# Optimization experiments

Hardware: AMD Instinct MI355X
Metric: run time of the kernel (lower is better)

## Reference

```python
import math
import jax, jax.numpy as jnp
import numpy as np

EPS = 1e-6
M, B, K, D, DZ = 4, 2048, 32, 256, 128

def setup_inputs() -> dict:
    key = jax.random.key(0)
    ks = jax.random.split(key, 8)
    return {
        "h_nei": jax.random.normal(ks[0], (M, B, K, D), jnp.float32),
        "ew_anc": jax.random.uniform(ks[1], (B, K, M), jnp.float32),
        "view_mask": jnp.ones((B, K, M), jnp.float32),
        "z_anc": jax.random.normal(ks[2], (B, DZ), jnp.float32),
        "lbl_delta": jax.random.normal(ks[3], (B, K, M, D), jnp.float32),
        "lbl_weight": jax.random.normal(ks[4], (B, K, M), jnp.float32) * 0.1,
        "W_Q": jax.random.normal(ks[5], (DZ, D), jnp.float32) / math.sqrt(DZ),
        "W_K": jax.random.normal(ks[6], (M, D, D), jnp.float32) / math.sqrt(D),
        "W_V": jax.random.normal(ks[7], (M, D, D), jnp.float32) / math.sqrt(D),
        "log_vw": jnp.zeros((M,), jnp.float32),
    }

def reference(h_nei, ew_anc, view_mask, z_anc, lbl_delta, lbl_weight, W_Q, W_K, W_V, log_vw):
    # Cross-attention mode (use_query_z=True). Dropout is identity (eval mode).
    d = h_nei.shape[-1]
    Q = z_anc @ W_Q                                            # [B, d]
    Kx = jnp.einsum('mbkd,mde->mbke', h_nei, W_K)              # [M, B, K, d]
    Vx = jnp.einsum('mbkd,mde->mbke', h_nei, W_V)
    Vx = Vx + jnp.moveaxis(lbl_delta, 2, 0)                    # add lbl_delta[:,:,m,:]
    ew = jnp.moveaxis(ew_anc, 2, 0)                            # [M, B, K]
    lw = jnp.moveaxis(lbl_weight, 2, 0)
    vm = jnp.moveaxis(view_mask, 2, 0)
    scores = jnp.einsum('bd,mbkd->mbk', Q, Kx) / math.sqrt(d)
    scores = scores + jnp.log(ew + EPS) + lw
    scores = jnp.where(vm == 0, -1e9, scores)
    attn = jax.nn.softmax(scores, axis=-1)                     # [M, B, K]
    ctx_m = jnp.einsum('mbk,mbkd->mbd', attn, Vx)              # [M, B, d]
    vw = jax.nn.softmax(log_vw)                                # [M]
    return jnp.einsum('m,mbd->bd', vw, ctx_m)                  # [B, d]
```

## Files before the change

kernel.cpp:

```cpp
#include <hip/hip_runtime.h>
#include <hip/hip_bf16.h>
#include <math.h>

#define M_  4
#define B_  2048
#define K_  32
#define D_  256
#define DZ_ 128
#define PAD 68

__global__ void __launch_bounds__(256) k0_wqk(const float* __restrict__ W_Q,
                                              const float* __restrict__ W_K,
                                              float* __restrict__ Wqk) {
    int mz = blockIdx.x;
    int m = mz >> 7, z = mz & 127;
    int d = threadIdx.x;
    __shared__ float wq[D_];
    wq[d] = W_Q[z * D_ + d];
    __syncthreads();
    const float* wk = W_K + (m * D_ + d) * D_;
    float acc = 0.f;
#pragma unroll 8
    for (int e = 0; e < D_; ++e) acc = fmaf(wq[e], wk[e], acc);
    Wqk[(m * DZ_ + z) * D_ + d] = acc;
}

__global__ void __launch_bounds__(256) k1_qk(const float* __restrict__ z_anc,
                                             const float* __restrict__ Wqk,
                                             float* __restrict__ Qk) {
    int m = blockIdx.z;
    int b0 = blockIdx.x * 64, d0 = blockIdx.y * 64;
    int t = threadIdx.x, tx = t & 15, ty = t >> 4;
    __shared__ float As[64 * PAD];
    __shared__ float Bs[64 * PAD];
    float c[4][4] = {};
    for (int kc = 0; kc < DZ_; kc += 64) {
#pragma unroll
        for (int it = 0; it < 4; ++it) {
            int s = it * 256 + t, bi = s >> 4, k4 = (s & 15) * 4;
            *(float4*)&As[bi * PAD + k4] =
                *(const float4*)&z_anc[(b0 + bi) * DZ_ + kc + k4];
        }
#pragma unroll
        for (int it = 0; it < 4; ++it) {
            int s = it * 256 + t, kk = s >> 4, d4 = (s & 15) * 4;
            *(float4*)&Bs[kk * PAD + d4] =
                *(const float4*)&Wqk[(m * DZ_ + kc + kk) * D_ + d0 + d4];
        }
        __syncthreads();
#pragma unroll 4
        for (int kk = 0; kk < 64; ++kk) {
            float a[4];
#pragma unroll
            for (int i = 0; i < 4; ++i) a[i] = As[(ty * 4 + i) * PAD + kk];
            float4 b4 = *(const float4*)&Bs[kk * PAD + tx * 4];
#pragma unroll
            for (int i = 0; i < 4; ++i) {
                c[i][0] = fmaf(a[i], b4.x, c[i][0]);
                c[i][1] = fmaf(a[i], b4.y, c[i][1]);
                c[i][2] = fmaf(a[i], b4.z, c[i][2]);
                c[i][3] = fmaf(a[i], b4.w, c[i][3]);
            }
        }
        __syncthreads();
    }
#pragma unroll
    for (int i = 0; i < 4; ++i) {
        float4 v = make_float4(c[i][0], c[i][1], c[i][2], c[i][3]);
        *(float4*)&Qk[(m * B_ + b0 + ty * 4 + i) * D_ + d0 + tx * 4] = v;
    }
}

__global__ void __launch_bounds__(256) k2_main(
    const float* __restrict__ h_nei, const float* __restrict__ ew_anc,
    const float* __restrict__ vmask, const float* __restrict__ lbl_delta,
    const float* __restrict__ lbl_w, const float* __restrict__ Qk,
    const float* __restrict__ log_vw,
    float* __restrict__ hbar, float* __restrict__ out)
{
    int b = blockIdx.x;
    int t = threadIdx.x;
    int w = t >> 6, l = t & 63;
    __shared__ float hs[K_ * D_];
    __shared__ float sc[K_], adj[K_], at[K_];

    float lv[4] = {log_vw[0], log_vw[1], log_vw[2], log_vw[3]};
    float mv = fmaxf(fmaxf(lv[0], lv[1]), fmaxf(lv[2], lv[3]));
    float ex[4], den = 0.f;
#pragma unroll
    for (int i = 0; i < 4; ++i) { ex[i] = expf(lv[i] - mv); den += ex[i]; }
    float vw[4];
#pragma unroll
    for (int i = 0; i < 4; ++i) vw[i] = ex[i] / den;

    float acc_ld = 0.f;
    for (int m = 0; m < M_; ++m) {
        __syncthreads();
        const float* hb = h_nei + (m * B_ + b) * (K_ * D_);
        float4 q4 = *(const float4*)&Qk[(m * B_ + b) * D_ + 4 * l];
        float accs[8];
#pragma unroll
        for (int i = 0; i < 8; ++i) {
            int s = i * 256 + t;
            float4 h4 = *(const float4*)&hb[4 * s];
            *(float4*)&hs[4 * s] = h4;
            accs[i] = h4.x * q4.x + h4.y * q4.y + h4.z * q4.z + h4.w * q4.w;
        }
#pragma unroll
        for (int i = 0; i < 8; ++i) {
            float v = accs[i];
            v += __shfl_xor(v, 32); v += __shfl_xor(v, 16); v += __shfl_xor(v, 8);
            v += __shfl_xor(v, 4);  v += __shfl_xor(v, 2);  v += __shfl_xor(v, 1);
            if (l == 0) sc[i * 4 + w] = v;
        }
        __syncthreads();
        if (t < K_) {
            int idx = (b * K_ + t) * M_ + m;
            float s = sc[t] * 0.0625f + logf(ew_anc[idx] + 1e-6f) + lbl_w[idx];
            if (vmask[idx] == 0.f) s = -1e9f;
            adj[t] = s;
        }
        __syncthreads();
        float mx = -3.4e38f;
        for (int k = 0; k < K_; ++k) mx = fmaxf(mx, adj[k]);
        float dsum = 0.f;
        for (int k = 0; k < K_; ++k) dsum += expf(adj[k] - mx);
        if (t < K_) at[t] = expf(adj[t] - mx) / dsum;
        __syncthreads();
        float ah = 0.f;
#pragma unroll 8
        for (int k = 0; k < K_; ++k) ah = fmaf(at[k], hs[k * D_ + t], ah);
        hbar[(m * B_ + b) * D_ + t] = vw[m] * ah;
        const float* ldp = lbl_delta + b * (K_ * M_ * D_) + m * D_;
        float vwm = vw[m];
#pragma unroll 8
        for (int k = 0; k < K_; ++k)
            acc_ld = fmaf(vwm * at[k], ldp[k * (M_ * D_) + t], acc_ld);
    }
    out[b * D_ + t] = acc_ld;
}

__global__ void __launch_bounds__(256) k3_gemm(const float* __restrict__ hbar,
                                               const float* __restrict__ W_V,
                                               float* __restrict__ out) {
    int m = blockIdx.z;
    int b0 = blockIdx.x * 64, e0 = blockIdx.y * 64;
    int t = threadIdx.x, tx = t & 15, ty = t >> 4;
    __shared__ float As[64 * PAD];
    __shared__ float Bs[64 * PAD];
    float c[4][4] = {};
    for (int kc = 0; kc < D_; kc += 64) {
#pragma unroll
        for (int it = 0; it < 4; ++it) {
            int s = it * 256 + t, bi = s >> 4, k4 = (s & 15) * 4;
            *(float4*)&As[bi * PAD + k4] =
                *(const float4*)&hbar[(m * B_ + b0 + bi) * D_ + kc + k4];
        }
#pragma unroll
        for (int it = 0; it < 4; ++it) {
            int s = it * 256 + t, kk = s >> 4, e4 = (s & 15) * 4;
            *(float4*)&Bs[kk * PAD + e4] =
                *(const float4*)&W_V[(m * D_ + kc + kk) * D_ + e0 + e4];
        }
        __syncthreads();
#pragma unroll 4
        for (int kk = 0; kk < 64; ++kk) {
            float a[4];
#pragma unroll
            for (int i = 0; i < 4; ++i) a[i] = As[(ty * 4 + i) * PAD + kk];
            float4 b4 = *(const float4*)&Bs[kk * PAD + tx * 4];
#pragma unroll
            for (int i = 0; i < 4; ++i) {
                c[i][0] = fmaf(a[i], b4.x, c[i][0]);
                c[i][1] = fmaf(a[i], b4.y, c[i][1]);
                c[i][2] = fmaf(a[i], b4.z, c[i][2]);
                c[i][3] = fmaf(a[i], b4.w, c[i][3]);
            }
        }
        __syncthreads();
    }
#pragma unroll
    for (int i = 0; i < 4; ++i)
#pragma unroll
        for (int j = 0; j < 4; ++j)
            atomicAdd(&out[(b0 + ty * 4 + i) * D_ + e0 + tx * 4 + j], c[i][j]);
}

extern "C" void kernel_launch(void* const* d_in, const int* in_sizes, int n_in,
                              void* d_out, int out_size, void* d_ws, size_t ws_size,
                              hipStream_t stream) {
    const float* h_nei     = (const float*)d_in[0];
    const float* ew_anc    = (const float*)d_in[1];
    const float* vmask     = (const float*)d_in[2];
    const float* z_anc     = (const float*)d_in[3];
    const float* lbl_delta = (const float*)d_in[4];
    const float* lbl_w     = (const float*)d_in[5];
    const float* W_Q       = (const float*)d_in[6];
    const float* W_K       = (const float*)d_in[7];
    const float* W_V       = (const float*)d_in[8];
    const float* log_vw    = (const float*)d_in[9];
    float* out = (float*)d_out;

    float* ws   = (float*)d_ws;
    float* Wqk  = ws;
    float* Qk   = ws + (M_ * DZ_ * D_);
    float* hbar = ws + (M_ * DZ_ * D_) + (M_ * B_ * D_);

    k0_wqk<<<M_ * DZ_, 256, 0, stream>>>(W_Q, W_K, Wqk);

    dim3 g1(B_ / 64, D_ / 64, M_);
    k1_qk<<<g1, 256, 0, stream>>>(z_anc, Wqk, Qk);

    k2_main<<<B_, 256, 0, stream>>>(h_nei, ew_anc, vmask, lbl_delta, lbl_w,
                                    Qk, log_vw, hbar, out);

    dim3 g3(B_ / 64, D_ / 64, M_);
    k3_gemm<<<g3, 256, 0, stream>>>(hbar, W_V, out);
}
```

Measured before the change: 189.8 us.

## Split main kernel across views, keep neighbor tile in registers, relayout hbar

After: 219.2 us. 1.16x slower.

```diff
diff --git a/kernel.cpp b/kernel.cpp
--- a/kernel.cpp
+++ b/kernel.cpp
@@ -78,89 +78,104 @@
     const float* __restrict__ log_vw,
     float* __restrict__ hbar, float* __restrict__ out)
 {
-    int b = blockIdx.x;
+    int b = blockIdx.x, m = blockIdx.y;
     int t = threadIdx.x;
     int w = t >> 6, l = t & 63;
-    __shared__ float hs[K_ * D_];
-    __shared__ float sc[K_], adj[K_], at[K_];
-
-    float lv[4] = {log_vw[0], log_vw[1], log_vw[2], log_vw[3]};
-    float mv = fmaxf(fmaxf(lv[0], lv[1]), fmaxf(lv[2], lv[3]));
-    float ex[4], den = 0.f;
-#pragma unroll
-    for (int i = 0; i < 4; ++i) { ex[i] = expf(lv[i] - mv); den += ex[i]; }
-    float vw[4];
-#pragma unroll
-    for (int i = 0; i < 4; ++i) vw[i] = ex[i] / den;
-
-    float acc_ld = 0.f;
-    for (int m = 0; m < M_; ++m) {
-        __syncthreads();
-        const float* hb = h_nei + (m * B_ + b) * (K_ * D_);
-        float4 q4 = *(const float4*)&Qk[(m * B_ + b) * D_ + 4 * l];
-        float accs[8];
-#pragma unroll
-        for (int i = 0; i < 8; ++i) {
-            int s = i * 256 + t;
-            float4 h4 = *(const float4*)&hb[4 * s];
-            *(float4*)&hs[4 * s] = h4;
-            accs[i] = h4.x * q4.x + h4.y * q4.y + h4.z * q4.z + h4.w * q4.w;
-        }
-#pragma unroll
-        for (int i = 0; i < 8; ++i) {
-            float v = accs[i];
-            v += __shfl_xor(v, 32); v += __shfl_xor(v, 16); v += __shfl_xor(v, 8);
-            v += __shfl_xor(v, 4);  v += __shfl_xor(v, 2);  v += __shfl_xor(v, 1);
-            if (l == 0) sc[i * 4 + w] = v;
-        }
-        __syncthreads();
-        if (t < K_) {
-            int idx = (b * K_ + t) * M_ + m;
-            float s = sc[t] * 0.0625f + logf(ew_anc[idx] + 1e-6f) + lbl_w[idx];
-            if (vmask[idx] == 0.f) s = -1e9f;
-            adj[t] = s;
-        }
-        __syncthreads();
-        float mx = -3.4e38f;
-        for (int k = 0; k < K_; ++k) mx = fmaxf(mx, adj[k]);
-        float dsum = 0.f;
-        for (int k = 0; k < K_; ++k) dsum += expf(adj[k] - mx);
-        if (t < K_) at[t] = expf(adj[t] - mx) / dsum;
-        __syncthreads();
-        float ah = 0.f;
+    __shared__ float sc[K_];
+    __shared__ float at[K_];
+    __shared__ float part[4 * D_];
+
+    float lv0 = log_vw[0], lv1 = log_vw[1], lv2 = log_vw[2], lv3 = log_vw[3];
+    float mv = fmaxf(fmaxf(lv0, lv1), fmaxf(lv2, lv3));
+    float e0 = expf(lv0 - mv), e1 = expf(lv1 - mv),
+          e2 = expf(lv2 - mv), e3 = expf(lv3 - mv);
+    float vw_m = ((m == 0) ? e0 : (m == 1) ? e1 : (m == 2) ? e2 : e3)
+                 / (e0 + e1 + e2 + e3);
+
+    float adjv = 0.f, vmv = 1.f;
+    if (t < K_) {
+        int idx = (b * K_ + t) * M_ + m;
+        adjv = logf(ew_anc[idx] + 1e-6f) + lbl_w[idx];
+        vmv = vmask[idx];
+    }
+
+    const float* hb = h_nei + ((size_t)(m * B_ + b)) * (K_ * D_);
+    float4 q4 = *(const float4*)&Qk[(m * B_ + b) * D_ + 4 * l];
+    float4 h4[8];
+    float accs[8];
+#pragma unroll
+    for (int i = 0; i < 8; ++i) {
+        int s = i * 256 + t;
+        h4[i] = *(const float4*)&hb[4 * s];
+        accs[i] = h4[i].x * q4.x + h4[i].y * q4.y + h4[i].z * q4.z + h4[i].w * q4.w;
+    }
+#pragma unroll
+    for (int i = 0; i < 8; ++i) {
+        float v = accs[i];
+        v += __shfl_xor(v, 32); v += __shfl_xor(v, 16); v += __shfl_xor(v, 8);
+        v += __shfl_xor(v, 4);  v += __shfl_xor(v, 2);  v += __shfl_xor(v, 1);
+        if (l == 0) sc[i * 4 + w] = v;
+    }
+    __syncthreads();
+
+    if (t < K_) {
+        float s = (vmv == 0.f) ? -1e9f : sc[t] * 0.0625f + adjv;
+        float mx = s;
+        mx = fmaxf(mx, __shfl_xor(mx, 16)); mx = fmaxf(mx, __shfl_xor(mx, 8));
+        mx = fmaxf(mx, __shfl_xor(mx, 4));  mx = fmaxf(mx, __shfl_xor(mx, 2));
+        mx = fmaxf(mx, __shfl_xor(mx, 1));
+        float ee = expf(s - mx);
+        float ds = ee;
+        ds += __shfl_xor(ds, 16); ds += __shfl_xor(ds, 8); ds += __shfl_xor(ds, 4);
+        ds += __shfl_xor(ds, 2);  ds += __shfl_xor(ds, 1);
+        at[t] = (ee / ds) * vw_m;
+    }
+    __syncthreads();
+
+    float4 p4 = make_float4(0.f, 0.f, 0.f, 0.f);
+#pragma unroll
+    for (int i = 0; i < 8; ++i) {
+        float a = at[i * 4 + w];
+        p4.x = fmaf(a, h4[i].x, p4.x);
+        p4.y = fmaf(a, h4[i].y, p4.y);
+        p4.z = fmaf(a, h4[i].z, p4.z);
+        p4.w = fmaf(a, h4[i].w, p4.w);
+    }
+    *(float4*)&part[w * D_ + 4 * l] = p4;
+
+    const float* ldp = lbl_delta + (size_t)b * (K_ * M_ * D_) + m * D_;
+    float acc = 0.f;
 #pragma unroll 8
-        for (int k = 0; k < K_; ++k) ah = fmaf(at[k], hs[k * D_ + t], ah);
-        hbar[(m * B_ + b) * D_ + t] = vw[m] * ah;
-        const float* ldp = lbl_delta + b * (K_ * M_ * D_) + m * D_;
-        float vwm = vw[m];
-#pragma unroll 8
-        for (int k = 0; k < K_; ++k)
-            acc_ld = fmaf(vwm * at[k], ldp[k * (M_ * D_) + t], acc_ld);
-    }
-    out[b * D_ + t] = acc_ld;
+    for (int k = 0; k < K_; ++k)
+        acc = fmaf(at[k], ldp[k * (M_ * D_) + t], acc);
+    atomicAdd(&out[b * D_ + t], acc);
+    __syncthreads();
+
+    float hv = part[t] + part[D_ + t] + part[2 * D_ + t] + part[3 * D_ + t];
+    hbar[(size_t)b * (M_ * D_) + m * D_ + t] = hv;
 }
 
 __global__ void __launch_bounds__(256) k3_gemm(const float* __restrict__ hbar,
                                                const float* __restrict__ W_V,
                                                float* __restrict__ out) {
-    int m = blockIdx.z;
     int b0 = blockIdx.x * 64, e0 = blockIdx.y * 64;
+    int kc0 = blockIdx.z * 128;
     int t = threadIdx.x, tx = t & 15, ty = t >> 4;
     __shared__ float As[64 * PAD];
     __shared__ float Bs[64 * PAD];
     float c[4][4] = {};
-    for (int kc = 0; kc < D_; kc += 64) {
+    for (int kc = kc0; kc < kc0 + 128; kc += 64) {
 #pragma unroll
         for (int it = 0; it < 4; ++it) {
             int s = it * 256 + t, bi = s >> 4, k4 = (s & 15) * 4;
             *(float4*)&As[bi * PAD + k4] =
-                *(const float4*)&hbar[(m * B_ + b0 + bi) * D_ + kc + k4];
+                *(const float4*)&hbar[(size_t)(b0 + bi) * (M_ * D_) + kc + k4];
         }
 #pragma unroll
         for (int it = 0; it < 4; ++it) {
             int s = it * 256 + t, kk = s >> 4, e4 = (s & 15) * 4;
             *(float4*)&Bs[kk * PAD + e4] =
-                *(const float4*)&W_V[(m * D_ + kc + kk) * D_ + e0 + e4];
+                *(const float4*)&W_V[(size_t)(kc + kk) * D_ + e0 + e4];
         }
         __syncthreads();
 #pragma unroll 4
@@ -206,14 +221,17 @@
     float* Qk   = ws + (M_ * DZ_ * D_);
     float* hbar = ws + (M_ * DZ_ * D_) + (M_ * B_ * D_);
 
+    hipMemsetAsync(out, 0, (size_t)B_ * D_ * sizeof(float), stream);
+
     k0_wqk<<<M_ * DZ_, 256, 0, stream>>>(W_Q, W_K, Wqk);
 
     dim3 g1(B_ / 64, D_ / 64, M_);
     k1_qk<<<g1, 256, 0, stream>>>(z_anc, Wqk, Qk);
 
-    k2_main<<<B_, 256, 0, stream>>>(h_nei, ew_anc, vmask, lbl_delta, lbl_w,
+    dim3 g2(B_, M_);
+    k2_main<<<g2, 256, 0, stream>>>(h_nei, ew_anc, vmask, lbl_delta, lbl_w,
                                     Qk, log_vw, hbar, out);
 
-    dim3 g3(B_ / 64, D_ / 64, M_);
+    dim3 g3(B_ / 64, D_ / 64, M_ * D_ / 128);
     k3_gemm<<<g3, 256, 0, stream>>>(hbar, W_V, out);
 }
```
